# Performance work log

Hardware: AMD Instinct MI355X
Metric: run time of the kernel (lower is better)

## Reference

```python
import jax, jax.numpy as jnp
import numpy as np


def setup_inputs() -> dict:
    key = jax.random.key(0)
    # Uniform in (0.9, 1.1) so the running product over 8192 elements stays finite.
    x = jax.random.uniform(key, (4096, 8192), dtype=jnp.float32, minval=0.9, maxval=1.1)
    return {"x": x}


def reference(x) -> jnp.ndarray:
    # Inclusive prefix product along dim 1 (matches cumprod_dim1_cuda / torch.cumprod(x, dim=1)).
    return jnp.cumprod(x, axis=1)
```

## Files before the change

kernel.cpp:

```cpp
#include <hip/hip_runtime.h>


#define N      8192
#define T      512
#define CHUNK  (N / T)
#define PADN   (N + (N / 32))
#define NW     (T / 64)

__device__ __forceinline__ int pidx(int e) { return e + (e >> 5); }

__global__ __launch_bounds__(T) void cumprod_rows_kernel(
    const float* __restrict__ x, float* __restrict__ out, int n_rows)
{
    __shared__ float lds[PADN];
    __shared__ float wsum[NW];

    const int row = blockIdx.x;
    if (row >= n_rows) return;
    const int tid = threadIdx.x;

    const float* __restrict__ xr   = x   + (size_t)row * N;
    float*       __restrict__ outr = out + (size_t)row * N;

#pragma unroll
    for (int v = 0; v < N / (T * 4); ++v) {
        const int e  = (v * T + tid) * 4;
        const float4 d = *reinterpret_cast<const float4*>(xr + e);
        const int pe = pidx(e);
        lds[pe + 0] = d.x; lds[pe + 1] = d.y;
        lds[pe + 2] = d.z; lds[pe + 3] = d.w;
    }
    __syncthreads();

    const int pbase = pidx(tid * CHUNK);
    float vals[CHUNK];
    float p = 1.0f;
#pragma unroll
    for (int j = 0; j < CHUNK; ++j) {
        p *= lds[pbase + j];
        vals[j] = p;
    }

    const int lane = tid & 63;
    const int wid  = tid >> 6;

    float inc = p;
#pragma unroll
    for (int off = 1; off < 64; off <<= 1) {
        const float o = __shfl_up(inc, off, 64);
        if (lane >= off) inc *= o;
    }
    if (lane == 63) wsum[wid] = inc;
    __syncthreads();

    float wpre = 1.0f;
#pragma unroll
    for (int w = 0; w < NW - 1; ++w)
        if (w < wid) wpre *= wsum[w];

    float excl = __shfl_up(inc, 1, 64);
    if (lane == 0) excl = 1.0f;
    excl *= wpre;

#pragma unroll
    for (int j = 0; j < CHUNK; ++j) lds[pbase + j] = vals[j] * excl;
    __syncthreads();

#pragma unroll
    for (int v = 0; v < N / (T * 4); ++v) {
        const int e  = (v * T + tid) * 4;
        const int pe = pidx(e);
        float4 d;
        d.x = lds[pe + 0]; d.y = lds[pe + 1];
        d.z = lds[pe + 2]; d.w = lds[pe + 3];
        *reinterpret_cast<float4*>(outr + e) = d;
    }
}

extern "C" void kernel_launch(void* const* d_in, const int* in_sizes, int n_in,
                              void* d_out, int out_size, void* d_ws, size_t ws_size,
                              hipStream_t stream)
{
    const float* x   = (const float*)d_in[0];
    float*       out = (float*)d_out;
    const int n_rows = in_sizes[0] / N;
    cumprod_rows_kernel<<<n_rows, T, 0, stream>>>(x, out, n_rows);
}
```

Baseline: 230.1 us.

## Replace LDS transpose with per-wave register scan over contiguous segments

Each wave now owns a contiguous 1024-element segment of the row. It loads float4s straight into registers, scans within each float4, and runs a wave-level shuffle scan per vector group with a running carry, so the padded LDS staging buffer and two of the barriers go away. Outputs are written with nontemporal stores. In exchange there are four shuffle scans per thread instead of one, which adds more serial shuffle latency.

```diff
diff --git a/kernel.cpp b/kernel.cpp
--- a/kernel.cpp
+++ b/kernel.cpp
@@ -3,54 +3,50 @@
 
 #define N      8192
 #define T      512
-#define CHUNK  (N / T)
-#define PADN   (N + (N / 32))
 #define NW     (T / 64)
+#define QV     (N / (T * 4))
 
-__device__ __forceinline__ int pidx(int e) { return e + (e >> 5); }
+typedef float f32x4 __attribute__((ext_vector_type(4)));
 
 __global__ __launch_bounds__(T) void cumprod_rows_kernel(
     const float* __restrict__ x, float* __restrict__ out, int n_rows)
 {
-    __shared__ float lds[PADN];
     __shared__ float wsum[NW];
 
     const int row = blockIdx.x;
     if (row >= n_rows) return;
-    const int tid = threadIdx.x;
-
-    const float* __restrict__ xr   = x   + (size_t)row * N;
-    float*       __restrict__ outr = out + (size_t)row * N;
-
-#pragma unroll
-    for (int v = 0; v < N / (T * 4); ++v) {
-        const int e  = (v * T + tid) * 4;
-        const float4 d = *reinterpret_cast<const float4*>(xr + e);
-        const int pe = pidx(e);
-        lds[pe + 0] = d.x; lds[pe + 1] = d.y;
-        lds[pe + 2] = d.z; lds[pe + 3] = d.w;
-    }
-    __syncthreads();
-
-    const int pbase = pidx(tid * CHUNK);
-    float vals[CHUNK];
-    float p = 1.0f;
-#pragma unroll
-    for (int j = 0; j < CHUNK; ++j) {
-        p *= lds[pbase + j];
-        vals[j] = p;
-    }
-
+    const int tid  = threadIdx.x;
     const int lane = tid & 63;
     const int wid  = tid >> 6;
 
-    float inc = p;
+    const float* __restrict__ xr   = x   + (size_t)row * N + (size_t)wid * (N / NW);
+    float*       __restrict__ outr = out + (size_t)row * N + (size_t)wid * (N / NW);
+
+    f32x4 d[QV];
 #pragma unroll
-    for (int off = 1; off < 64; off <<= 1) {
-        const float o = __shfl_up(inc, off, 64);
-        if (lane >= off) inc *= o;
+    for (int v = 0; v < QV; ++v)
+        d[v] = *reinterpret_cast<const f32x4*>(xr + (v * 64 + lane) * 4);
+
+    float carry = 1.0f;
+    float coef[QV];
+#pragma unroll
+    for (int v = 0; v < QV; ++v) {
+        d[v].y *= d[v].x;
+        d[v].z *= d[v].y;
+        d[v].w *= d[v].z;
+        float inc = d[v].w;
+#pragma unroll
+        for (int off = 1; off < 64; off <<= 1) {
+            const float o = __shfl_up(inc, off, 64);
+            if (lane >= off) inc *= o;
+        }
+        float ex = __shfl_up(inc, 1, 64);
+        if (lane == 0) ex = 1.0f;
+        coef[v] = carry * ex;
+        carry  *= __shfl(inc, 63, 64);
     }
-    if (lane == 63) wsum[wid] = inc;
+
+    if (lane == 63) wsum[wid] = carry;
     __syncthreads();
 
     float wpre = 1.0f;
@@ -58,22 +54,12 @@
     for (int w = 0; w < NW - 1; ++w)
         if (w < wid) wpre *= wsum[w];
 
-    float excl = __shfl_up(inc, 1, 64);
-    if (lane == 0) excl = 1.0f;
-    excl *= wpre;
-
 #pragma unroll
-    for (int j = 0; j < CHUNK; ++j) lds[pbase + j] = vals[j] * excl;
-    __syncthreads();
-
-#pragma unroll
-    for (int v = 0; v < N / (T * 4); ++v) {
-        const int e  = (v * T + tid) * 4;
-        const int pe = pidx(e);
-        float4 d;
-        d.x = lds[pe + 0]; d.y = lds[pe + 1];
-        d.z = lds[pe + 2]; d.w = lds[pe + 3];
-        *reinterpret_cast<float4*>(outr + e) = d;
+    for (int v = 0; v < QV; ++v) {
+        const float f = wpre * coef[v];
+        f32x4 o = d[v];
+        o.x *= f; o.y *= f; o.z *= f; o.w *= f;
+        __builtin_nontemporal_store(o, reinterpret_cast<f32x4*>(outr + (v * 64 + lane) * 4));
     }
 }
 
```

New measurement: 231.6 us. No clear change (+0.6%).
